# Optimization experiments

Measured on AMD Instinct MI355X. Metric: run time of the kernel, lower is better.

The kernel has to match this reference:

```python
import jax, jax.numpy as jnp
import numpy as np

B, N, F_IN, F_OUT = 8, 4096, 256, 256


def setup_inputs() -> dict:
    key = jax.random.key(0)
    k1, k2, k3 = jax.random.split(key, 3)
    H = jax.random.normal(k1, (B, N, F_IN), dtype=jnp.float32)
    W = jax.random.normal(k2, (F_IN, F_OUT), dtype=jnp.float32) * (1.0 / np.sqrt(F_IN))
    A = jax.random.normal(k3, (N, N), dtype=jnp.float32) * (1.414 * np.sqrt(2.0 / (N + N)))
    return {"H": H, "W": W, "A": A}


def reference(H, W, A):
    # HW: [B, N, F_out]
    HW = jnp.einsum('bnf,fo->bno', H, W)
    # symmetrize + relu -> nonneg adjacency [N, N]
    A_norm = jax.nn.relu((A + A.T) * 0.5)
    # degree and inverse sqrt (inf -> 0 for isolated nodes)
    D = jnp.sum(A_norm, axis=1)
    D_safe = jnp.where(D > 0, D, 1.0)
    d_inv_sqrt = jnp.where(D > 0, D_safe ** -0.5, 0.0)
    # L_norm = I - D^{-1/2} A D^{-1/2}  (diagonal scaling, no dense diag matmul)
    DAD = d_inv_sqrt[:, None] * A_norm * d_inv_sqrt[None, :]
    L_norm = jnp.eye(N, dtype=H.dtype) - DAD
    # output = relu(L_norm @ HW): [B, N, F_out]
    out = jnp.einsum('nm,bmo->bno', L_norm, HW)
    return jax.nn.relu(out)
```

## Files before the change

### kernel.cpp

```cpp
#include <hip/hip_runtime.h>
#include <stdint.h>

#define N_NODES 4096
#define F_DIM   256
#define BATCH   8

typedef __attribute__((ext_vector_type(8))) __bf16 bf16x8;
typedef __attribute__((ext_vector_type(4))) float  f32x4;
typedef __attribute__((ext_vector_type(8))) unsigned short u16x8;

typedef const __attribute__((address_space(1))) void* gas1_t;
typedef __attribute__((address_space(3))) void*       las3_t;

__device__ __forceinline__ void stage16(const void* g, void* l) {
  __builtin_amdgcn_global_load_lds((gas1_t)g, (las3_t)l, 16, 0, 0);
}

__device__ __forceinline__ unsigned short f2bf(float f) {
  union { float f; uint32_t u; } v; v.f = f;
  uint32_t u = v.u;
  return (unsigned short)((u + 0x7FFFu + ((u >> 16) & 1u)) >> 16);
}
__device__ __forceinline__ float bf2f(unsigned short u) {
  union { uint32_t u; float f; } v; v.u = ((uint32_t)u) << 16;
  return v.f;
}

__global__ __launch_bounds__(256) void k_sym(const float* __restrict__ A,
                                             unsigned short* __restrict__ Sb,
                                             float* __restrict__ D) {
  int bi = blockIdx.y, bj = blockIdx.x;
  if (bj < bi) return;
  __shared__ float L1[64][65];
  __shared__ float L2[64][65];
  __shared__ float Pr[4][64];
  __shared__ float Pc[4][64];
  int t = threadIdx.x;
  int i0 = bi * 64, j0 = bj * 64;
  for (int it = 0; it < 16; ++it) {
    int idx = it * 256 + t;
    int r = idx >> 6, c = idx & 63;
    L1[r][c] = A[(size_t)(i0 + r) * N_NODES + (j0 + c)];
    L2[c][r] = A[(size_t)(j0 + r) * N_NODES + (i0 + c)];
  }
  __syncthreads();
  float colsum = 0.f;
  int cfix = t & 63, q = t >> 6;
  for (int it = 0; it < 16; ++it) {
    int r = it * 4 + q;
    float v = 0.5f * (L1[r][cfix] + L2[r][cfix]);
    v = v > 0.f ? v : 0.f;
    Sb[(size_t)(i0 + r) * N_NODES + (j0 + cfix)] = f2bf(v);
    colsum += v;
    L1[r][cfix] = v;
  }
  Pc[q][cfix] = colsum;
  __syncthreads();
  {
    int r = t & 63, seg = t >> 6;
    float s = 0.f;
    for (int c = seg * 16; c < seg * 16 + 16; ++c) s += L1[r][c];
    Pr[seg][r] = s;
  }
  __syncthreads();
  if (t < 64) {
    float d = Pr[0][t] + Pr[1][t] + Pr[2][t] + Pr[3][t];
    atomicAdd(&D[i0 + t], d);
  } else if (t < 128 && bi != bj) {
    int c = t - 64;
    float d = Pc[0][c] + Pc[1][c] + Pc[2][c] + Pc[3][c];
    atomicAdd(&D[j0 + c], d);
  }
  if (bi != bj) {
    for (int it = 0; it < 16; ++it) {
      int idx = it * 256 + t;
      int ro = idx >> 6, co = idx & 63;
      Sb[(size_t)(j0 + ro) * N_NODES + (i0 + co)] = f2bf(L1[co][ro]);
    }
  }
}

__global__ void k_dinv(const float* __restrict__ D, float* __restrict__ dinv) {
  int i = blockIdx.x * blockDim.x + threadIdx.x;
  if (i < N_NODES) {
    float d = D[i];
    dinv[i] = d > 0.f ? 1.0f / sqrtf(d) : 0.f;
  }
}

__global__ __launch_bounds__(256) void k_cvt(const float4* __restrict__ H,
                                             ushort4* __restrict__ Hb,
                                             const float* __restrict__ W,
                                             unsigned short* __restrict__ Wt) {
  int bid = blockIdx.x;
  if (bid < 8192) {
    int i = bid * 256 + threadIdx.x;
    float4 v = H[i];
    ushort4 o;
    o.x = f2bf(v.x); o.y = f2bf(v.y); o.z = f2bf(v.z); o.w = f2bf(v.w);
    Hb[i] = o;
  } else {
    int t = (bid - 8192) * 256 + threadIdx.x;
    int f = t >> 8, o = t & 255;
    Wt[o * 256 + f] = f2bf(W[t]);
  }
}

__global__ __launch_bounds__(256) void k_gemm1(const unsigned short* __restrict__ Hb,
                                               const unsigned short* __restrict__ Wt,
                                               const float* __restrict__ dinv,
                                               unsigned short* __restrict__ HWb,
                                               unsigned short* __restrict__ Gt) {
  __shared__ __align__(16) unsigned short As[128 * 32];
  __shared__ __align__(16) unsigned short Bs[128 * 32];
  __shared__ __align__(16) unsigned short T[128][136];
  int t = threadIdx.x;
  int lane = t & 63;
  int q = lane >> 4, r16 = lane & 15;
  int wave = t >> 6;
  int wm = wave >> 1, wn = wave & 1;
  int m0 = blockIdx.y * 128;
  int o0 = blockIdx.x * 128;
  const int K = 256;

  const unsigned short* Abase = Hb + (size_t)m0 * K;
  const unsigned short* Bbase = Wt + (size_t)o0 * K;

  f32x4 acc[4][4];
#pragma unroll
  for (int i = 0; i < 4; ++i)
#pragma unroll
    for (int j = 0; j < 4; ++j) acc[i][j] = f32x4{0.f, 0.f, 0.f, 0.f};

  int idx0 = t, idx1 = 256 + t;
  int wb0 = (t & ~63) * 8;
  int wb1 = (256 + (t & ~63)) * 8;

  for (int kt = 0; kt < K / 32; ++kt) {
    int kof = kt * 32;
    stage16(Abase + (size_t)(idx0 >> 2) * K + kof + ((idx0 & 3) << 3), &As[wb0]);
    stage16(Abase + (size_t)(idx1 >> 2) * K + kof + ((idx1 & 3) << 3), &As[wb1]);
    stage16(Bbase + (size_t)(idx0 >> 2) * K + kof + ((idx0 & 3) << 3), &Bs[wb0]);
    stage16(Bbase + (size_t)(idx1 >> 2) * K + kof + ((idx1 & 3) << 3), &Bs[wb1]);
    __syncthreads();
    bf16x8 a[4], b[4];
#pragma unroll
    for (int mi = 0; mi < 4; ++mi)
      a[mi] = *(const bf16x8*)&As[(wm * 64 + mi * 16 + r16) * 32 + q * 8];
#pragma unroll
    for (int ni = 0; ni < 4; ++ni)
      b[ni] = *(const bf16x8*)&Bs[(wn * 64 + ni * 16 + r16) * 32 + q * 8];
#pragma unroll
    for (int mi = 0; mi < 4; ++mi)
#pragma unroll
      for (int ni = 0; ni < 4; ++ni)
        acc[mi][ni] = __builtin_amdgcn_mfma_f32_16x16x32_bf16(a[mi], b[ni], acc[mi][ni], 0, 0, 0);
    __syncthreads();
  }

#pragma unroll
  for (int mi = 0; mi < 4; ++mi) {
    int row = wm * 64 + mi * 16 + q * 4;
#pragma unroll
    for (int ni = 0; ni < 4; ++ni) {
      int col = wn * 64 + ni * 16 + r16;
#pragma unroll
      for (int rr = 0; rr < 4; ++rr) {
        unsigned short h = f2bf(acc[mi][ni][rr]);
        HWb[(size_t)(m0 + row + rr) * F_DIM + (o0 + col)] = h;
        T[col][row + rr] = h;
      }
    }
  }
  __syncthreads();
  int b = m0 >> 12, n0 = m0 & 4095;
  for (int it = 0; it < 8; ++it) {
    int unit = it * 256 + t;
    int ro = unit >> 4;
    int cs = (unit & 15) * 8;
    u16x8 v = *(const u16x8*)&T[ro][cs];
    u16x8 w;
#pragma unroll
    for (int j = 0; j < 8; ++j)
      w[j] = f2bf(bf2f(v[j]) * dinv[n0 + cs + j]);
    *(u16x8*)&Gt[(size_t)(b * 256 + o0 + ro) * N_NODES + n0 + cs] = w;
  }
}

__global__ __launch_bounds__(256) void k_gemm2(const unsigned short* __restrict__ Sb,
                                               const unsigned short* __restrict__ Gt,
                                               const unsigned short* __restrict__ HWb,
                                               const float* __restrict__ dinv,
                                               float* __restrict__ Out) {
  __shared__ __align__(16) unsigned short As[2][128 * 32];
  __shared__ __align__(16) unsigned short Bs[2][128 * 32];
  const int K = N_NODES;
  int t = threadIdx.x;
  int lane = t & 63;
  int q = lane >> 4, r16 = lane & 15;
  int wave = t >> 6;
  int wm = wave >> 1, wn = wave & 1;
  int m0 = blockIdx.y * 128;
  int n0 = blockIdx.x * 128;

  const unsigned short* Abase = Sb + (size_t)m0 * K;
  const unsigned short* Bbase = Gt + (size_t)n0 * K;

  f32x4 acc[4][4];
#pragma unroll
  for (int i = 0; i < 4; ++i)
#pragma unroll
    for (int j = 0; j < 4; ++j) acc[i][j] = f32x4{0.f, 0.f, 0.f, 0.f};

  int idx0 = t, idx1 = 256 + t;
  int wb0 = (t & ~63) * 8;
  int wb1 = (256 + (t & ~63)) * 8;
  size_t ga0 = (size_t)(idx0 >> 2) * K + ((idx0 & 3) << 3);
  size_t ga1 = (size_t)(idx1 >> 2) * K + ((idx1 & 3) << 3);

#define STG(kt, bb)                                        \
  {                                                        \
    int kof = (kt) * 32;                                   \
    stage16(Abase + ga0 + kof, &As[bb][wb0]);              \
    stage16(Abase + ga1 + kof, &As[bb][wb1]);              \
    stage16(Bbase + ga0 + kof, &Bs[bb][wb0]);              \
    stage16(Bbase + ga1 + kof, &Bs[bb][wb1]);              \
  }

  STG(0, 0)
  for (int kt = 0; kt < K / 32; ++kt) {
    int cur = kt & 1;
    __syncthreads();
    if (kt + 1 < K / 32) STG(kt + 1, cur ^ 1)
    bf16x8 a[4], b[4];
#pragma unroll
    for (int mi = 0; mi < 4; ++mi)
      a[mi] = *(const bf16x8*)&As[cur][(wm * 64 + mi * 16 + r16) * 32 + q * 8];
#pragma unroll
    for (int ni = 0; ni < 4; ++ni)
      b[ni] = *(const bf16x8*)&Bs[cur][(wn * 64 + ni * 16 + r16) * 32 + q * 8];
#pragma unroll
    for (int mi = 0; mi < 4; ++mi)
#pragma unroll
      for (int ni = 0; ni < 4; ++ni)
        acc[mi][ni] = __builtin_amdgcn_mfma_f32_16x16x32_bf16(a[mi], b[ni], acc[mi][ni], 0, 0, 0);
  }
#undef STG

#pragma unroll
  for (int mi = 0; mi < 4; ++mi) {
    int row = m0 + wm * 64 + mi * 16 + q * 4;
    float di[4];
#pragma unroll
    for (int rr = 0; rr < 4; ++rr) di[rr] = dinv[row + rr];
#pragma unroll
    for (int ni = 0; ni < 4; ++ni) {
      int col = n0 + wn * 64 + ni * 16 + r16;
      int b_ = col >> 8, o = col & 255;
#pragma unroll
      for (int rr = 0; rr < 4; ++rr) {
        size_t oi = ((size_t)b_ * N_NODES + (row + rr)) * F_DIM + o;
        float u = bf2f(HWb[oi]) - di[rr] * acc[mi][ni][rr];
        Out[oi] = u > 0.f ? u : 0.f;
      }
    }
  }
}

extern "C" void kernel_launch(void* const* d_in, const int* in_sizes, int n_in,
                              void* d_out, int out_size, void* d_ws, size_t ws_size,
                              hipStream_t stream) {
  (void)in_sizes; (void)n_in; (void)out_size; (void)ws_size;
  const float* H = (const float*)d_in[0];
  const float* W = (const float*)d_in[1];
  const float* A = (const float*)d_in[2];
  float* out = (float*)d_out;

  char* ws = (char*)d_ws;
  size_t off = 0;
  auto alloc = [&](size_t bytes) {
    char* p = ws + off;
    off += (bytes + 255) & ~(size_t)255;
    return p;
  };
  float*          Dd   = (float*)alloc((size_t)N_NODES * 4);
  float*          dinv = (float*)alloc((size_t)N_NODES * 4);
  unsigned short* Sb   = (unsigned short*)alloc((size_t)N_NODES * N_NODES * 2);
  unsigned short* HWb  = (unsigned short*)alloc((size_t)BATCH * N_NODES * F_DIM * 2);
  unsigned short* Gt   = (unsigned short*)alloc((size_t)BATCH * F_DIM * N_NODES * 2);
  unsigned short* Wt   = (unsigned short*)alloc((size_t)F_DIM * F_DIM * 2);
  unsigned short* Hb   = (unsigned short*)alloc((size_t)BATCH * N_NODES * F_DIM * 2);

  hipMemsetAsync(Dd, 0, N_NODES * 4, stream);
  k_sym<<<dim3(64, 64), 256, 0, stream>>>(A, Sb, Dd);
  k_dinv<<<16, 256, 0, stream>>>(Dd, dinv);
  k_cvt<<<8448, 256, 0, stream>>>((const float4*)H, (ushort4*)Hb, W, Wt);
  k_gemm1<<<dim3(2, 256), 256, 0, stream>>>(Hb, Wt, dinv, HWb, Gt);
  k_gemm2<<<dim3(16, 32), 256, 0, stream>>>(Sb, Gt, HWb, dinv, out);
}
```

Measured before the change: 266.8 us.

## Fuse H/W conversion into symmetrize kernel and split K across waves in gemm2

The H and W bf16 conversion moves into the symmetrization kernel, which removes one launch, and every block converts a slice before the early return. In gemm2, each wave now computes a 64x128 tile. Pairs of waves alternate K-steps (split-K inside the block) and are summed through an LDS reduction buffer, with an XOR-style swizzle on LDS staging to cut bank conflicts. This drops the double buffering and adds two barriers per K step, so half the waves sit idle each step, in exchange for larger per-wave tiles and fewer LDS reads per MFMA.

```diff
diff --git a/kernel.cpp b/kernel.cpp
--- a/kernel.cpp
+++ b/kernel.cpp
@@ -26,16 +26,33 @@
   return v.f;
 }
 
-__global__ __launch_bounds__(256) void k_sym(const float* __restrict__ A,
+__global__ __launch_bounds__(256) void k_pre(const float* __restrict__ A,
                                              unsigned short* __restrict__ Sb,
-                                             float* __restrict__ D) {
+                                             float* __restrict__ D,
+                                             const float4* __restrict__ H4,
+                                             ushort4* __restrict__ Hb4,
+                                             const float* __restrict__ W,
+                                             unsigned short* __restrict__ Wt) {
+  int t = threadIdx.x;
+  int bid = blockIdx.y * 64 + blockIdx.x;
+  {
+    int i = bid * 512 + t;
+    float4 v = H4[i];
+    ushort4 o; o.x = f2bf(v.x); o.y = f2bf(v.y); o.z = f2bf(v.z); o.w = f2bf(v.w);
+    Hb4[i] = o;
+    i += 256;
+    v = H4[i];
+    o.x = f2bf(v.x); o.y = f2bf(v.y); o.z = f2bf(v.z); o.w = f2bf(v.w);
+    Hb4[i] = o;
+  }
+  if (bid < 256) Wt[t * 256 + bid] = f2bf(W[bid * 256 + t]);
+
   int bi = blockIdx.y, bj = blockIdx.x;
   if (bj < bi) return;
   __shared__ float L1[64][65];
   __shared__ float L2[64][65];
   __shared__ float Pr[4][64];
   __shared__ float Pc[4][64];
-  int t = threadIdx.x;
   int i0 = bi * 64, j0 = bj * 64;
   for (int it = 0; it < 16; ++it) {
     int idx = it * 256 + t;
@@ -85,24 +102,6 @@
   if (i < N_NODES) {
     float d = D[i];
     dinv[i] = d > 0.f ? 1.0f / sqrtf(d) : 0.f;
-  }
-}
-
-__global__ __launch_bounds__(256) void k_cvt(const float4* __restrict__ H,
-                                             ushort4* __restrict__ Hb,
-                                             const float* __restrict__ W,
-                                             unsigned short* __restrict__ Wt) {
-  int bid = blockIdx.x;
-  if (bid < 8192) {
-    int i = bid * 256 + threadIdx.x;
-    float4 v = H[i];
-    ushort4 o;
-    o.x = f2bf(v.x); o.y = f2bf(v.y); o.z = f2bf(v.z); o.w = f2bf(v.w);
-    Hb[i] = o;
-  } else {
-    int t = (bid - 8192) * 256 + threadIdx.x;
-    int f = t >> 8, o = t & 255;
-    Wt[o * 256 + f] = f2bf(W[t]);
   }
 }
 
@@ -187,83 +186,110 @@
   }
 }
 
-__global__ __launch_bounds__(256) void k_gemm2(const unsigned short* __restrict__ Sb,
-                                               const unsigned short* __restrict__ Gt,
-                                               const unsigned short* __restrict__ HWb,
-                                               const float* __restrict__ dinv,
-                                               float* __restrict__ Out) {
-  __shared__ __align__(16) unsigned short As[2][128 * 32];
-  __shared__ __align__(16) unsigned short Bs[2][128 * 32];
+__global__ __launch_bounds__(256, 2) void k_gemm2(const unsigned short* __restrict__ Sb,
+                                                  const unsigned short* __restrict__ Gt,
+                                                  const unsigned short* __restrict__ HWb,
+                                                  const float* __restrict__ dinv,
+                                                  float* __restrict__ Out) {
+  __shared__ __align__(16) unsigned short As[128 * 32];
+  __shared__ __align__(16) unsigned short Bs[128 * 32];
+  __shared__ float Red[64 * 130];
   const int K = N_NODES;
   int t = threadIdx.x;
   int lane = t & 63;
   int q = lane >> 4, r16 = lane & 15;
   int wave = t >> 6;
-  int wm = wave >> 1, wn = wave & 1;
+  int wm = wave >> 1;
+  int kz = wave & 1;
   int m0 = blockIdx.y * 128;
   int n0 = blockIdx.x * 128;
 
   const unsigned short* Abase = Sb + (size_t)m0 * K;
   const unsigned short* Bbase = Gt + (size_t)n0 * K;
 
-  f32x4 acc[4][4];
+  f32x4 acc[4][8];
 #pragma unroll
   for (int i = 0; i < 4; ++i)
 #pragma unroll
-    for (int j = 0; j < 4; ++j) acc[i][j] = f32x4{0.f, 0.f, 0.f, 0.f};
-
-  int idx0 = t, idx1 = 256 + t;
+    for (int j = 0; j < 8; ++j) acc[i][j] = f32x4{0.f, 0.f, 0.f, 0.f};
+
+  int u0 = t, u1 = 256 + t;
+  int r0 = u0 >> 2, q0 = ((u0 & 3) - (r0 >> 1)) & 3;
+  int r1 = u1 >> 2, q1 = ((u1 & 3) - (r1 >> 1)) & 3;
+  const unsigned short* pa0 = Abase + (size_t)r0 * K + q0 * 8;
+  const unsigned short* pa1 = Abase + (size_t)r1 * K + q1 * 8;
+  const unsigned short* pb0 = Bbase + (size_t)r0 * K + q0 * 8;
+  const unsigned short* pb1 = Bbase + (size_t)r1 * K + q1 * 8;
   int wb0 = (t & ~63) * 8;
   int wb1 = (256 + (t & ~63)) * 8;
-  size_t ga0 = (size_t)(idx0 >> 2) * K + ((idx0 & 3) << 3);
-  size_t ga1 = (size_t)(idx1 >> 2) * K + ((idx1 & 3) << 3);
-
-#define STG(kt, bb)                                        \
-  {                                                        \
-    int kof = (kt) * 32;                                   \
-    stage16(Abase + ga0 + kof, &As[bb][wb0]);              \
-    stage16(Abase + ga1 + kof, &As[bb][wb1]);              \
-    stage16(Bbase + ga0 + kof, &Bs[bb][wb0]);              \
-    stage16(Bbase + ga1 + kof, &Bs[bb][wb1]);              \
-  }
-
-  STG(0, 0)
+
+  int aoff[4], boff[8];
+#pragma unroll
+  for (int mi = 0; mi < 4; ++mi) {
+    int row = wm * 64 + mi * 16 + r16;
+    aoff[mi] = row * 32 + (((q + (row >> 1)) & 3) << 3);
+  }
+#pragma unroll
+  for (int ni = 0; ni < 8; ++ni) {
+    int row = ni * 16 + r16;
+    boff[ni] = row * 32 + (((q + (row >> 1)) & 3) << 3);
+  }
+
   for (int kt = 0; kt < K / 32; ++kt) {
-    int cur = kt & 1;
-    __syncthreads();
-    if (kt + 1 < K / 32) STG(kt + 1, cur ^ 1)
-    bf16x8 a[4], b[4];
-#pragma unroll
-    for (int mi = 0; mi < 4; ++mi)
-      a[mi] = *(const bf16x8*)&As[cur][(wm * 64 + mi * 16 + r16) * 32 + q * 8];
-#pragma unroll
-    for (int ni = 0; ni < 4; ++ni)
-      b[ni] = *(const bf16x8*)&Bs[cur][(wn * 64 + ni * 16 + r16) * 32 + q * 8];
-#pragma unroll
-    for (int mi = 0; mi < 4; ++mi)
-#pragma unroll
-      for (int ni = 0; ni < 4; ++ni)
-        acc[mi][ni] = __builtin_amdgcn_mfma_f32_16x16x32_bf16(a[mi], b[ni], acc[mi][ni], 0, 0, 0);
-  }
-#undef STG
-
-#pragma unroll
-  for (int mi = 0; mi < 4; ++mi) {
-    int row = m0 + wm * 64 + mi * 16 + q * 4;
-    float di[4];
-#pragma unroll
-    for (int rr = 0; rr < 4; ++rr) di[rr] = dinv[row + rr];
-#pragma unroll
-    for (int ni = 0; ni < 4; ++ni) {
-      int col = n0 + wn * 64 + ni * 16 + r16;
-      int b_ = col >> 8, o = col & 255;
-#pragma unroll
-      for (int rr = 0; rr < 4; ++rr) {
-        size_t oi = ((size_t)b_ * N_NODES + (row + rr)) * F_DIM + o;
-        float u = bf2f(HWb[oi]) - di[rr] * acc[mi][ni][rr];
-        Out[oi] = u > 0.f ? u : 0.f;
+    int kof = kt * 32;
+    stage16(pa0 + kof, &As[wb0]);
+    stage16(pa1 + kof, &As[wb1]);
+    stage16(pb0 + kof, &Bs[wb0]);
+    stage16(pb1 + kof, &Bs[wb1]);
+    __syncthreads();
+    if ((kt & 1) == kz) {
+      bf16x8 a[4], b[8];
+#pragma unroll
+      for (int mi = 0; mi < 4; ++mi) a[mi] = *(const bf16x8*)&As[aoff[mi]];
+#pragma unroll
+      for (int ni = 0; ni < 8; ++ni) b[ni] = *(const bf16x8*)&Bs[boff[ni]];
+#pragma unroll
+      for (int mi = 0; mi < 4; ++mi)
+#pragma unroll
+        for (int ni = 0; ni < 8; ++ni)
+          acc[mi][ni] = __builtin_amdgcn_mfma_f32_16x16x32_bf16(a[mi], b[ni], acc[mi][ni], 0, 0, 0);
+    }
+    __syncthreads();
+  }
+
+  for (int round = 0; round < 2; ++round) {
+    if (wm == round && kz == 1) {
+#pragma unroll
+      for (int mi = 0; mi < 4; ++mi)
+#pragma unroll
+        for (int ni = 0; ni < 8; ++ni)
+#pragma unroll
+          for (int rr = 0; rr < 4; ++rr)
+            Red[(mi * 16 + q * 4 + rr) * 130 + ni * 16 + r16] = acc[mi][ni][rr];
+    }
+    __syncthreads();
+    if (wm == round && kz == 0) {
+#pragma unroll
+      for (int mi = 0; mi < 4; ++mi) {
+        int row = m0 + wm * 64 + mi * 16 + q * 4;
+        float di[4];
+#pragma unroll
+        for (int rr = 0; rr < 4; ++rr) di[rr] = dinv[row + rr];
+#pragma unroll
+        for (int ni = 0; ni < 8; ++ni) {
+          int col = n0 + ni * 16 + r16;
+          int b_ = col >> 8, o = col & 255;
+#pragma unroll
+          for (int rr = 0; rr < 4; ++rr) {
+            float v = acc[mi][ni][rr] + Red[(mi * 16 + q * 4 + rr) * 130 + ni * 16 + r16];
+            size_t oi = ((size_t)b_ * N_NODES + (row + rr)) * F_DIM + o;
+            float u = bf2f(HWb[oi]) - di[rr] * v;
+            Out[oi] = u > 0.f ? u : 0.f;
+          }
+        }
       }
     }
+    __syncthreads();
   }
 }
 
@@ -292,9 +318,8 @@
   unsigned short* Hb   = (unsigned short*)alloc((size_t)BATCH * N_NODES * F_DIM * 2);
 
   hipMemsetAsync(Dd, 0, N_NODES * 4, stream);
-  k_sym<<<dim3(64, 64), 256, 0, stream>>>(A, Sb, Dd);
+  k_pre<<<dim3(64, 64), 256, 0, stream>>>(A, Sb, Dd, (const float4*)H, (ushort4*)Hb, W, Wt);
   k_dinv<<<16, 256, 0, stream>>>(Dd, dinv);
-  k_cvt<<<8448, 256, 0, stream>>>((const float4*)H, (ushort4*)Hb, W, Wt);
   k_gemm1<<<dim3(2, 256), 256, 0, stream>>>(Hb, Wt, dinv, HWb, Gt);
   k_gemm2<<<dim3(16, 32), 256, 0, stream>>>(Sb, Gt, HWb, dinv, out);
 }
```

Result: faster. 260.0 us (-2.6%).
